# Kernel optimization log

Hardware: AMD Instinct MI355X
Metric: run time of the kernel (lower is better)

## Reference

```python
import jax, jax.numpy as jnp
import numpy as np

V, EMB, H, N, E, B = 100000, 300, 64, 20000, 160000, 4096
L, T = 2, 3  # layer_timesteps = [3, 3]


def setup_inputs() -> dict:
    key = jax.random.key(0)
    ks = jax.random.split(key, 24)
    ri = lambda k, shape, hi: jax.random.randint(k, shape, 0, hi)
    rn = lambda k, shape, s=0.05: (jax.random.normal(k, shape, dtype=jnp.float32) * s)
    emb_table = rn(ks[7], (V, EMB), 0.1).at[0].set(0.0)  # padding_idx=0 row is zeros
    return {
        'emb_ind0': ri(ks[0], (N,), V),
        'emb_ind1': ri(ks[1], (N,), V),
        'adj0': ri(ks[2], (E, 2), N),
        'adj1': ri(ks[3], (E, 2), N),
        'prop_ind0': ri(ks[4], (B,), N),
        'prop_ind1': ri(ks[5], (B,), N),
        'labels': ri(ks[6], (B,), 2),
        'emb_table': emb_table,
        'proj_W': rn(ks[8], (EMB, H)),   # emb_proj weight (stored input-major)
        'proj_b': jnp.zeros((H,), jnp.float32),
        'msg_W': rn(ks[9], (L, H, H)),   # per-layer edge-type-0 message linear
        'msg_b': jnp.zeros((L, H), jnp.float32),
        'gru_Wih': rn(ks[10], (L, 3 * H, H)),
        'gru_Whh': rn(ks[11], (L, 3 * H, H)),
        'gru_bih': jnp.zeros((L, 3 * H), jnp.float32),
        'gru_bhh': jnp.zeros((L, 3 * H), jnp.float32),
        'cla_W1': rn(ks[12], (2 * H, 16)),
        'cla_b1': jnp.zeros((16,), jnp.float32),
        'cla_W2': rn(ks[13], (16, 1)),
        'cla_b2': jnp.zeros((1,), jnp.float32),
    }


def _gru_cell(x, h, Wih, Whh, bih, bhh):
    # torch.nn.GRUCell math
    gi = x @ Wih.T + bih
    gh = h @ Whh.T + bhh
    i_r, i_z, i_n = jnp.split(gi, 3, axis=-1)
    h_r, h_z, h_n = jnp.split(gh, 3, axis=-1)
    r = jax.nn.sigmoid(i_r + h_r)
    z = jax.nn.sigmoid(i_z + h_z)
    n = jnp.tanh(i_n + r * h_n)
    return (1.0 - z) * n + z * h


def reference(emb_ind0, emb_ind1, adj0, adj1, prop_ind0, prop_ind1, labels,
              emb_table, proj_W, proj_b, msg_W, msg_b,
              gru_Wih, gru_Whh, gru_bih, gru_bhh,
              cla_W1, cla_b1, cla_W2, cla_b2):
    def ggnn(x, adj):
        src, tgt = adj[:, 0], adj[:, 1]
        h = x
        for l in range(L):              # 2 structurally distinct layers
            for _ in range(T):          # 3 timesteps each
                m = h[src] @ msg_W[l] + msg_b[l]                     # [E, H] gather + transform
                inc = jax.ops.segment_sum(m, tgt, num_segments=N)    # scatter-add messages
                h = _gru_cell(inc, h, gru_Wih[l], gru_Whh[l], gru_bih[l], gru_bhh[l])
        return h

    def branch(emb_ind, adj, prop_ind):
        ge = emb_table[emb_ind]          # embedding lookup [N, EMB]
        ge = ge @ proj_W + proj_b        # emb_proj -> [N, H]
        ge = ggnn(ge, adj)
        return ge[prop_ind]              # index_select -> [B, H]

    g0 = branch(emb_ind0, adj0, prop_ind0)
    g1 = branch(emb_ind1, adj1, prop_ind1)
    ge = jnp.concatenate([g0, g1], axis=-1)                 # match='concat' -> [B, 2H]
    hid = jax.nn.relu(ge @ cla_W1 + cla_b1)
    logits = jax.nn.sigmoid(hid @ cla_W2 + cla_b2)          # [B, 1], num_class=1 path
    p = logits.squeeze(-1)
    y = labels.astype(p.dtype)
    eps = 1e-7  # mirrors torch BCELoss log-clamping
    loss = -jnp.mean(y * jnp.log(jnp.clip(p, eps, 1.0))
                     + (1.0 - y) * jnp.log(jnp.clip(1.0 - p, eps, 1.0)))
    return logits, loss
```

## Files before the change

kernel.cpp:

```cpp
#include <hip/hip_runtime.h>
#include <hip/hip_bf16.h>

typedef unsigned short u16;
typedef __attribute__((ext_vector_type(8))) short s16x8;
typedef __attribute__((ext_vector_type(4))) float f32x4;

#define NN 20000
#define HH 64
#define EMBD 300
#define EE 160000
#define BB 4096
#define NODES 40000
#define SLST  640000

#define OFF_PROJB 0
#define OFF_MSGB  64
#define OFF_BIH   192
#define OFF_BHH   576
#define OFF_CW1T  960
#define OFF_CB1   3008
#define OFF_CW2   3024
#define OFF_CB2   3040
#define PARAM_SZ  3072

#define PB_WIH   0
#define PB_WHH   24576
#define PB_WMT   49152
#define PB_PROJT 57344
#define PB_SZ    77824

#define APAD 344

__device__ __forceinline__ float b2f(u16 u) {
    union { unsigned int i; float f; } v; v.i = ((unsigned int)u) << 16; return v.f;
}
__device__ __forceinline__ u16 f2b(float f) {
    union { float f; unsigned int u; } v; v.f = f;
    unsigned int u = v.u;
    return (u16)((u + 0x7FFFu + ((u >> 16) & 1u)) >> 16);
}
__device__ __forceinline__ float ldf(const void* p, long long i, int isbf) {
    return isbf ? b2f(((const u16*)p)[i]) : ((const float*)p)[i];
}
__device__ __forceinline__ u16 ldb(const void* p, long long i, int isbf) {
    return isbf ? ((const u16*)p)[i] : f2b(((const float*)p)[i]);
}
__device__ __forceinline__ void stf(void* p, long long i, int isbf, float v) {
    if (isbf) ((u16*)p)[i] = f2b(v);
    else      ((float*)p)[i] = v;
}

__global__ void sniff_kernel(const u16* probe, int* flag)
{
    if (threadIdx.x == 0 && blockIdx.x == 0) {
        int good = 0;
        for (int i = 0; i < 128; i += 2) {
            unsigned int e = (probe[i] >> 7) & 0xFF;
            if (e >= 105 && e <= 127) good++;
        }
        *flag = (good >= 48) ? 1 : 0;
    }
}

__global__ __launch_bounds__(256) void conv_kernel(
    const void* projW, const void* projb, const void* msgW, const void* msgb,
    const void* wih, const void* whh, const void* bih, const void* bhh,
    const void* cw1, const void* cb1, const void* cw2, const void* cb2,
    float* P, u16* PB, const int* flag)
{
    int isbf = *flag;
    int i = blockIdx.x * 256 + threadIdx.x;
    if (i < 64)    P[OFF_PROJB + i] = ldf(projb, i, isbf);
    if (i < 128)   P[OFF_MSGB + i]  = ldf(msgb, i, isbf);
    if (i < 384)   { P[OFF_BIH + i] = ldf(bih, i, isbf); P[OFF_BHH + i] = ldf(bhh, i, isbf); }
    if (i < 2048)  { int t = i >> 7, k = i & 127; P[OFF_CW1T + i] = ldf(cw1, (long long)k * 16 + t, isbf); }
    if (i < 16)    { P[OFF_CB1 + i] = ldf(cb1, i, isbf); P[OFF_CW2 + i] = ldf(cw2, i, isbf); }
    if (i == 0)    P[OFF_CB2] = ldf(cb2, 0, isbf);

    if (i < 24576) {
        int l = i / 12288, r = i - l * 12288;
        int frag = r >> 9, rr = r & 511, lane = rr >> 3, e = rr & 7;
        int jt = frag >> 1, kt = frag & 1;
        int srow = jt * 16 + (lane & 15);
        int sk = kt * 32 + ((lane >> 4) << 3) + e;
        long long si = (long long)l * 12288 + srow * 64 + sk;
        PB[PB_WIH + i] = ldb(wih, si, isbf);
        PB[PB_WHH + i] = ldb(whh, si, isbf);
    }
    if (i < 8192) {
        int l = i >> 12, r = i & 4095;
        int frag = r >> 9, rr = r & 511, lane = rr >> 3, e = rr & 7;
        int jt = frag >> 1, kt = frag & 1;
        int srow = jt * 16 + (lane & 15);
        int sk = kt * 32 + ((lane >> 4) << 3) + e;
        PB[PB_WMT + i] = ldb(msgW, (long long)l * 4096 + sk * 64 + srow, isbf);
    }
    if (i < 20480) {
        int frag = i >> 9, rr = i & 511, lane = rr >> 3, e = rr & 7;
        int jt = frag / 10, kt = frag - jt * 10;
        int srow = jt * 16 + (lane & 15);
        int sk = kt * 32 + ((lane >> 4) << 3) + e;
        PB[PB_PROJT + i] = (sk < 300) ? ldb(projW, (long long)sk * 64 + srow, isbf) : (u16)0;
    }
}

__global__ __launch_bounds__(256) void hist_kernel(const int* __restrict__ adj0,
                                                   const int* __restrict__ adj1, int* off)
{
    int e = blockIdx.x * 256 + threadIdx.x;
    if (e >= 2 * EE) return;
    int b = e / EE, le = e - b * EE;
    const int* adj = b ? adj1 : adj0;
    int tgt = adj[2 * le + 1];
    atomicAdd(&off[b * (NN + 1) + tgt + 1], 1);
}

__global__ __launch_bounds__(1024) void scan_kernel(int* off, int* cursor)
{
    int b = blockIdx.x;
    int* o = off + (size_t)b * (NN + 1);
    int* cur = cursor + (size_t)b * NN;
    __shared__ int wsum[16];
    __shared__ int wscan[16];
    int tid = threadIdx.x, wv = tid >> 6, lane = tid & 63;
    int base = 0;
    for (int start = 0; start < NN; start += 1024) {
        int i = start + tid;
        int v = (i < NN) ? o[i + 1] : 0;
        int orig = v;
        #pragma unroll
        for (int d = 1; d < 64; d <<= 1) {
            int t = __shfl_up(v, d);
            if (lane >= d) v += t;
        }
        if (lane == 63) wsum[wv] = v;
        __syncthreads();
        if (tid < 16) {
            int w = wsum[tid];
            #pragma unroll
            for (int d = 1; d < 16; d <<= 1) {
                int t = __shfl_up(w, d, 16);
                if (tid >= d) w += t;
            }
            wscan[tid] = w;
        }
        __syncthreads();
        int woff = (wv == 0) ? 0 : wscan[wv - 1];
        int excl = base + woff + v - orig;
        if (i < NN) { o[i] = excl; cur[i] = excl; }
        base += wscan[15];
    }
    if (tid == 0) o[NN] = base;
}

__global__ __launch_bounds__(256) void scatter_kernel(const int* __restrict__ adj0,
                                                      const int* __restrict__ adj1,
                                                      int* cursor, int* esrc)
{
    int e = blockIdx.x * 256 + threadIdx.x;
    if (e >= 2 * EE) return;
    int b = e / EE, le = e - b * EE;
    const int* adj = b ? adj1 : adj0;
    int src = adj[2 * le + 0];
    int tgt = adj[2 * le + 1];
    int pos = atomicAdd(&cursor[b * NN + tgt], 1);
    esrc[(size_t)b * EE + pos] = src;
}

__global__ __launch_bounds__(256) void projm_kernel(const void* emb,
                                                    const int* __restrict__ i0,
                                                    const int* __restrict__ i1,
                                                    const float* __restrict__ P,
                                                    const u16* __restrict__ PB,
                                                    u16* __restrict__ h, const int* flag)
{
    __shared__ u16 sA[64 * APAD];
    int isbf = *flag;
    int tid = threadIdx.x;
    int node0 = blockIdx.x * 64;

    {
        int r = tid >> 2, sub = tid & 3;
        int n = node0 + r;
        int b = n >= NN;
        int ln = n - b * NN;
        int idx = b ? i1[ln] : i0[ln];
        if (isbf) {
            const ushort4* src = (const ushort4*)((const u16*)emb + (size_t)idx * EMBD);
            ushort4* dst = (ushort4*)(sA + r * APAD);
            for (int c = sub; c < 75; c += 4) dst[c] = src[c];
            if (sub == 0) {
                ushort4 z = {0, 0, 0, 0};
                for (int c = 75; c < 80; ++c) dst[c] = z;
            }
        } else {
            const float* src = (const float*)emb + (size_t)idx * EMBD;
            for (int k = sub; k < 300; k += 4) sA[r * APAD + k] = f2b(src[k]);
            if (sub == 0) for (int k = 300; k < 320; ++k) sA[r * APAD + k] = 0;
        }
    }

    int wv = tid >> 6, lane = tid & 63, quad = lane >> 4, cn = lane & 15;
    int m0 = wv * 16;
    f32x4 acc[4];
    #pragma unroll
    for (int j = 0; j < 4; ++j) {
        float bb = P[OFF_PROJB + j * 16 + cn];
        acc[j] = {bb, bb, bb, bb};
    }
    #pragma unroll
    for (int kt = 0; kt < 10; ++kt) {
        s16x8 a = *(const s16x8*)&sA[(m0 + cn) * APAD + kt * 32 + quad * 8];
        #pragma unroll
        for (int j = 0; j < 4; ++j) {
            s16x8 bfr = *(const s16x8*)&PB[PB_PROJT + (j * 10 + kt) * 512 + lane * 8];
            acc[j] = __builtin_amdgcn_mfma_f32_16x16x32_bf16(a, bfr, acc[j], 0, 0, 0);
        }
    }
    #pragma unroll
    for (int j = 0; j < 4; ++j)
        #pragma unroll
        for (int r = 0; r < 4; ++r)
            h[(size_t)j * SLST + (size_t)(node0 + m0 + quad * 4 + r) * 16 + cn] = f2b(acc[j][r]);
}

__global__ __launch_bounds__(256) void gatherS_kernel(const u16* __restrict__ h_old,
                                                      u16* __restrict__ Sbuf,
                                                      const int* __restrict__ ioff,
                                                      const int* __restrict__ esrc)
{
    int b = blockIdx.x;
    int slice = b & 3;
    int tile = b >> 2;
    int tid = threadIdx.x;
    int i = tid >> 4, feat = tid & 15;
    int node = tile * 16 + i;
    int br = node >= NN;
    int ln = node - br * NN;
    const int* o = ioff + (size_t)br * (NN + 1);
    int s0 = o[ln], s1 = o[ln + 1];
    const int* es = esrc + (size_t)br * EE;
    const u16* hb = h_old + (size_t)slice * SLST + (size_t)br * NN * 16;
    float a0 = 0.f, a1 = 0.f, a2 = 0.f, a3 = 0.f;
    int e = s0;
    for (; e + 4 <= s1; e += 4) {
        int e0 = es[e], e1 = es[e + 1], e2 = es[e + 2], e3 = es[e + 3];
        a0 += b2f(hb[(size_t)e0 * 16 + feat]);
        a1 += b2f(hb[(size_t)e1 * 16 + feat]);
        a2 += b2f(hb[(size_t)e2 * 16 + feat]);
        a3 += b2f(hb[(size_t)e3 * 16 + feat]);
    }
    for (; e < s1; ++e) a0 += b2f(hb[(size_t)es[e] * 16 + feat]);
    Sbuf[(size_t)slice * SLST + (size_t)node * 16 + feat] = f2b(a0 + a1 + a2 + a3);
}

__global__ __launch_bounds__(256) void gstep_kernel(const u16* __restrict__ Sbuf,
                                                    const u16* __restrict__ h_old,
                                                    u16* __restrict__ h_new,
                                                    const int* __restrict__ ioff,
                                                    const float* __restrict__ P,
                                                    const u16* __restrict__ PB, int l)
{
    __shared__ u16 s_S[4096];
    __shared__ u16 s_h[4096];
    __shared__ float s_deg[64];

    int tid = threadIdx.x;
    int wv = tid >> 6, lane = tid & 63;
    int node0 = blockIdx.x * 64;
    int m0 = wv * 16;

    #pragma unroll
    for (int it = 0; it < 2; ++it) {
        int idx = it * 64 + lane;
        int slice = idx >> 5;
        int rem = idx & 31;
        int nlo = rem >> 1, half = rem & 1;
        int row = m0 + nlo;
        size_t goff = (size_t)slice * SLST + (size_t)(node0 + row) * 16 + half * 8;
        *(uint4*)(s_h + row * 64 + slice * 16 + half * 8) = *(const uint4*)(h_old + goff);
        *(uint4*)(s_S + row * 64 + slice * 16 + half * 8) = *(const uint4*)(Sbuf + goff);
    }
    if (lane < 16) {
        int row = m0 + lane;
        int n = node0 + row;
        int br = n >= NN;
        int ln = n - br * NN;
        const int* o = ioff + (size_t)br * (NN + 1);
        s_deg[row] = (float)(o[ln + 1] - o[ln]);
    }

    int quad = lane >> 4, cn = lane & 15;
    int arow = (m0 + cn) * 64 + quad * 8;
    int fl = lane * 8;

    s16x8 aS0 = *(const s16x8*)&s_S[arow];
    s16x8 aS1 = *(const s16x8*)&s_S[arow + 32];
    const u16* WM = PB + PB_WMT + (size_t)l * 4096;
    #pragma unroll
    for (int jt = 0; jt < 4; ++jt) {
        float mb = P[OFF_MSGB + l * 64 + jt * 16 + cn];
        f32x4 acc;
        acc[0] = s_deg[m0 + quad * 4 + 0] * mb;
        acc[1] = s_deg[m0 + quad * 4 + 1] * mb;
        acc[2] = s_deg[m0 + quad * 4 + 2] * mb;
        acc[3] = s_deg[m0 + quad * 4 + 3] * mb;
        acc = __builtin_amdgcn_mfma_f32_16x16x32_bf16(aS0, *(const s16x8*)&WM[(jt * 2 + 0) * 512 + fl], acc, 0, 0, 0);
        acc = __builtin_amdgcn_mfma_f32_16x16x32_bf16(aS1, *(const s16x8*)&WM[(jt * 2 + 1) * 512 + fl], acc, 0, 0, 0);
        #pragma unroll
        for (int r = 0; r < 4; ++r)
            s_S[(m0 + quad * 4 + r) * 64 + jt * 16 + cn] = f2b(acc[r]);
    }

    s16x8 aI0 = *(const s16x8*)&s_S[arow];
    s16x8 aI1 = *(const s16x8*)&s_S[arow + 32];
    s16x8 aH0 = *(const s16x8*)&s_h[arow];
    s16x8 aH1 = *(const s16x8*)&s_h[arow + 32];
    const u16* WI = PB + PB_WIH + (size_t)l * 12288;
    const u16* WH = PB + PB_WHH + (size_t)l * 12288;
    const float* bi = P + OFF_BIH + l * 192;
    const float* bh = P + OFF_BHH + l * 192;

    #pragma unroll
    for (int c = 0; c < 4; ++c) {
        int j0 = c * 16;
        float vr = bi[j0 + cn], vz = bi[64 + j0 + cn], vn = bi[128 + j0 + cn];
        float wr = bh[j0 + cn], wz = bh[64 + j0 + cn], wn = bh[128 + j0 + cn];
        f32x4 gr = {vr, vr, vr, vr}, gz = {vz, vz, vz, vz}, gn = {vn, vn, vn, vn};
        f32x4 hr = {wr, wr, wr, wr}, hz = {wz, wz, wz, wz}, hn = {wn, wn, wn, wn};
        int fr = (c * 2) * 512 + fl, frz = ((4 + c) * 2) * 512 + fl, frn = ((8 + c) * 2) * 512 + fl;
        gr = __builtin_amdgcn_mfma_f32_16x16x32_bf16(aI0, *(const s16x8*)&WI[fr], gr, 0, 0, 0);
        gr = __builtin_amdgcn_mfma_f32_16x16x32_bf16(aI1, *(const s16x8*)&WI[fr + 512], gr, 0, 0, 0);
        gz = __builtin_amdgcn_mfma_f32_16x16x32_bf16(aI0, *(const s16x8*)&WI[frz], gz, 0, 0, 0);
        gz = __builtin_amdgcn_mfma_f32_16x16x32_bf16(aI1, *(const s16x8*)&WI[frz + 512], gz, 0, 0, 0);
        gn = __builtin_amdgcn_mfma_f32_16x16x32_bf16(aI0, *(const s16x8*)&WI[frn], gn, 0, 0, 0);
        gn = __builtin_amdgcn_mfma_f32_16x16x32_bf16(aI1, *(const s16x8*)&WI[frn + 512], gn, 0, 0, 0);
        hr = __builtin_amdgcn_mfma_f32_16x16x32_bf16(aH0, *(const s16x8*)&WH[fr], hr, 0, 0, 0);
        hr = __builtin_amdgcn_mfma_f32_16x16x32_bf16(aH1, *(const s16x8*)&WH[fr + 512], hr, 0, 0, 0);
        hz = __builtin_amdgcn_mfma_f32_16x16x32_bf16(aH0, *(const s16x8*)&WH[frz], hz, 0, 0, 0);
        hz = __builtin_amdgcn_mfma_f32_16x16x32_bf16(aH1, *(const s16x8*)&WH[frz + 512], hz, 0, 0, 0);
        hn = __builtin_amdgcn_mfma_f32_16x16x32_bf16(aH0, *(const s16x8*)&WH[frn], hn, 0, 0, 0);
        hn = __builtin_amdgcn_mfma_f32_16x16x32_bf16(aH1, *(const s16x8*)&WH[frn + 512], hn, 0, 0, 0);
        #pragma unroll
        for (int r = 0; r < 4; ++r) {
            int row = m0 + quad * 4 + r;
            float rr = 1.f / (1.f + __expf(-(gr[r] + hr[r])));
            float zz = 1.f / (1.f + __expf(-(gz[r] + hz[r])));
            float nn = tanhf(gn[r] + rr * hn[r]);
            float ho = b2f(s_h[row * 64 + j0 + cn]);
            h_new[(size_t)c * SLST + (size_t)(node0 + row) * 16 + cn] = f2b((1.f - zz) * nn + zz * ho);
        }
    }
}

__global__ __launch_bounds__(256) void cls_kernel(const u16* __restrict__ h,
                                                  const int* __restrict__ p0,
                                                  const int* __restrict__ p1,
                                                  const int* __restrict__ labels,
                                                  const float* __restrict__ P,
                                                  void* out, float* partial, const int* flag)
{
    int isbf = *flag;
    int wv = threadIdx.x >> 6, lane = threadIdx.x & 63;
    int s = blockIdx.x * 4 + wv;
    int n0 = p0[s], n1 = p1[s];
    size_t sl = (size_t)(lane >> 4) * SLST;
    float f0 = b2f(h[sl + (size_t)n0 * 16 + (lane & 15)]);
    float f1 = b2f(h[sl + (size_t)(NN + n1) * 16 + (lane & 15)]);
    float z = P[OFF_CB2];
    #pragma unroll
    for (int t = 0; t < 16; ++t) {
        float part = f0 * P[OFF_CW1T + t * 128 + lane] + f1 * P[OFF_CW1T + t * 128 + 64 + lane];
        #pragma unroll
        for (int off = 32; off; off >>= 1) part += __shfl_xor(part, off);
        z += fmaxf(part + P[OFF_CB1 + t], 0.f) * P[OFF_CW2 + t];
    }
    float p = 1.f / (1.f + expf(-z));
    float y = (float)labels[s];
    const float eps = 1e-7f;
    float pc  = fminf(fmaxf(p, eps), 1.f);
    float pc1 = fminf(fmaxf(1.f - p, eps), 1.f);
    float term = y * logf(pc) + (1.f - y) * logf(pc1);
    __shared__ float red[4];
    if (lane == 0) { stf(out, s, isbf, p); red[wv] = term; }
    __syncthreads();
    if (threadIdx.x == 0) partial[blockIdx.x] = red[0] + red[1] + red[2] + red[3];
}

__global__ __launch_bounds__(256) void loss_kernel(const float* __restrict__ partial,
                                                   void* out, const int* flag)
{
    __shared__ float red[256];
    int tid = threadIdx.x;
    float s = 0.f;
    for (int i = tid; i < 1024; i += 256) s += partial[i];
    red[tid] = s;
    __syncthreads();
    for (int d = 128; d > 0; d >>= 1) {
        if (tid < d) red[tid] += red[tid + d];
        __syncthreads();
    }
    if (tid == 0) stf(out, BB, *flag, -red[0] / (float)BB);
}

extern "C" void kernel_launch(void* const* d_in, const int* in_sizes, int n_in,
                              void* d_out, int out_size, void* d_ws, size_t ws_size,
                              hipStream_t stream)
{
    const int* adj0   = (const int*)d_in[2];
    const int* adj1   = (const int*)d_in[3];
    const int* prop0  = (const int*)d_in[4];
    const int* prop1  = (const int*)d_in[5];
    const int* labels = (const int*)d_in[6];

    int* flag = (int*)d_ws;
    float* P  = (float*)d_ws + 16;
    u16* PB   = (u16*)(P + PARAM_SZ);
    u16* h0   = PB + PB_SZ;
    u16* h1   = h0 + (size_t)4 * SLST / 4 * 4;
    u16* SB   = h1 + (size_t)2560000;
    float* partial = (float*)(SB + (size_t)2560000);
    int* ioff   = (int*)(partial + 1024);
    int* cursor = ioff + 2 * (NN + 1) + 62;
    int* esrc   = cursor + 2 * NN;

    hipMemsetAsync(ioff, 0, 2 * (NN + 1) * sizeof(int), stream);

    sniff_kernel<<<1, 64, 0, stream>>>((const u16*)d_in[8], flag);
    conv_kernel<<<96, 256, 0, stream>>>(d_in[8], d_in[9], d_in[10], d_in[11], d_in[12], d_in[13],
                                        d_in[14], d_in[15], d_in[16], d_in[17], d_in[18], d_in[19],
                                        P, PB, flag);
    hist_kernel<<<(2 * EE) / 256, 256, 0, stream>>>(adj0, adj1, ioff);
    scan_kernel<<<2, 1024, 0, stream>>>(ioff, cursor);
    scatter_kernel<<<(2 * EE) / 256, 256, 0, stream>>>(adj0, adj1, cursor, esrc);
    projm_kernel<<<(2 * NN) / 64, 256, 0, stream>>>(d_in[7], (const int*)d_in[0],
                                                    (const int*)d_in[1], P, PB, h0, flag);

    u16* hcur = h0;
    u16* hnext = h1;
    for (int l = 0; l < 2; ++l) {
        for (int t = 0; t < 3; ++t) {
            gatherS_kernel<<<4 * (NODES / 16), 256, 0, stream>>>(hcur, SB, ioff, esrc);
            gstep_kernel<<<NODES / 64, 256, 0, stream>>>(SB, hcur, hnext, ioff, P, PB, l);
            u16* tmp = hcur; hcur = hnext; hnext = tmp;
        }
    }

    cls_kernel<<<BB / 4, 256, 0, stream>>>(hcur, prop0, prop1, labels, P, d_out, partial, flag);
    loss_kernel<<<1, 256, 0, stream>>>(partial, d_out, flag);
}
```

Before: 464.8 us.

## Widen node-state slices to 32 features, stage GRU weights in LDS, fold memset

Node hidden states move from four 16-feature slices to two 32-feature slices, so each gathered neighbour row is a 64-byte read instead of 32 bytes, which halves the number of scattered gather transactions per edge. The gstep kernel now copies the per-layer Wih, Whh and message weights into shared memory before its MFMAs, and replaces tanhf with an exp-based formula. The hipMemset of the offset array is folded into the conversion kernel. The cost is about 57 KB of extra LDS per block, which lowers occupancy, plus a redundant weight copy in every block.

```diff
diff --git a/kernel.cpp b/kernel.cpp
--- a/kernel.cpp
+++ b/kernel.cpp
@@ -11,7 +11,7 @@
 #define EE 160000
 #define BB 4096
 #define NODES 40000
-#define SLST  640000
+#define SLST2 1280000
 
 #define OFF_PROJB 0
 #define OFF_MSGB  64
@@ -29,6 +29,10 @@
 #define PB_PROJT 57344
 #define PB_SZ    77824
 
+#define WIH_S 0
+#define WHH_S 12288
+#define WMT_S 24576
+
 #define APAD 344
 
 __device__ __forceinline__ float b2f(u16 u) {
@@ -66,10 +70,11 @@
     const void* projW, const void* projb, const void* msgW, const void* msgb,
     const void* wih, const void* whh, const void* bih, const void* bhh,
     const void* cw1, const void* cb1, const void* cw2, const void* cb2,
-    float* P, u16* PB, const int* flag)
+    float* P, u16* PB, int* ioff, const int* flag)
 {
     int isbf = *flag;
     int i = blockIdx.x * 256 + threadIdx.x;
+    if (i < 2 * (NN + 1)) ioff[i] = 0;
     if (i < 64)    P[OFF_PROJB + i] = ldf(projb, i, isbf);
     if (i < 128)   P[OFF_MSGB + i]  = ldf(msgb, i, isbf);
     if (i < 384)   { P[OFF_BIH + i] = ldf(bih, i, isbf); P[OFF_BHH + i] = ldf(bhh, i, isbf); }
@@ -221,7 +226,8 @@
     for (int j = 0; j < 4; ++j)
         #pragma unroll
         for (int r = 0; r < 4; ++r)
-            h[(size_t)j * SLST + (size_t)(node0 + m0 + quad * 4 + r) * 16 + cn] = f2b(acc[j][r]);
+            h[(size_t)(j >> 1) * SLST2 + (size_t)(node0 + m0 + quad * 4 + r) * 32
+              + (j & 1) * 16 + cn] = f2b(acc[j][r]);
 }
 
 __global__ __launch_bounds__(256) void gatherS_kernel(const u16* __restrict__ h_old,
@@ -230,28 +236,28 @@
                                                       const int* __restrict__ esrc)
 {
     int b = blockIdx.x;
-    int slice = b & 3;
-    int tile = b >> 2;
+    int slice = b & 1;
+    int tile = b >> 1;
     int tid = threadIdx.x;
-    int i = tid >> 4, feat = tid & 15;
-    int node = tile * 16 + i;
+    int i = tid >> 5, feat = tid & 31;
+    int node = tile * 8 + i;
     int br = node >= NN;
     int ln = node - br * NN;
     const int* o = ioff + (size_t)br * (NN + 1);
     int s0 = o[ln], s1 = o[ln + 1];
     const int* es = esrc + (size_t)br * EE;
-    const u16* hb = h_old + (size_t)slice * SLST + (size_t)br * NN * 16;
+    const u16* hb = h_old + (size_t)slice * SLST2 + (size_t)br * NN * 32;
     float a0 = 0.f, a1 = 0.f, a2 = 0.f, a3 = 0.f;
     int e = s0;
     for (; e + 4 <= s1; e += 4) {
         int e0 = es[e], e1 = es[e + 1], e2 = es[e + 2], e3 = es[e + 3];
-        a0 += b2f(hb[(size_t)e0 * 16 + feat]);
-        a1 += b2f(hb[(size_t)e1 * 16 + feat]);
-        a2 += b2f(hb[(size_t)e2 * 16 + feat]);
-        a3 += b2f(hb[(size_t)e3 * 16 + feat]);
-    }
-    for (; e < s1; ++e) a0 += b2f(hb[(size_t)es[e] * 16 + feat]);
-    Sbuf[(size_t)slice * SLST + (size_t)node * 16 + feat] = f2b(a0 + a1 + a2 + a3);
+        a0 += b2f(hb[(size_t)e0 * 32 + feat]);
+        a1 += b2f(hb[(size_t)e1 * 32 + feat]);
+        a2 += b2f(hb[(size_t)e2 * 32 + feat]);
+        a3 += b2f(hb[(size_t)e3 * 32 + feat]);
+    }
+    for (; e < s1; ++e) a0 += b2f(hb[(size_t)es[e] * 32 + feat]);
+    Sbuf[(size_t)slice * SLST2 + (size_t)node * 32 + feat] = f2b(a0 + a1 + a2 + a3);
 }
 
 __global__ __launch_bounds__(256) void gstep_kernel(const u16* __restrict__ Sbuf,
@@ -261,6 +267,7 @@
                                                     const float* __restrict__ P,
                                                     const u16* __restrict__ PB, int l)
 {
+    __shared__ u16 s_W[28672];
     __shared__ u16 s_S[4096];
     __shared__ u16 s_h[4096];
     __shared__ float s_deg[64];
@@ -270,16 +277,25 @@
     int node0 = blockIdx.x * 64;
     int m0 = wv * 16;
 
+    {
+        const uint4* a = (const uint4*)(PB + PB_WIH + (size_t)l * 12288);
+        const uint4* bq = (const uint4*)(PB + PB_WHH + (size_t)l * 12288);
+        uint4* da = (uint4*)(s_W + WIH_S);
+        uint4* db = (uint4*)(s_W + WHH_S);
+        for (int i = tid; i < 1536; i += 256) { da[i] = a[i]; db[i] = bq[i]; }
+        const uint4* cq = (const uint4*)(PB + PB_WMT + (size_t)l * 4096);
+        uint4* dc = (uint4*)(s_W + WMT_S);
+        for (int i = tid; i < 512; i += 256) dc[i] = cq[i];
+    }
+
     #pragma unroll
     for (int it = 0; it < 2; ++it) {
-        int idx = it * 64 + lane;
-        int slice = idx >> 5;
-        int rem = idx & 31;
-        int nlo = rem >> 1, half = rem & 1;
-        int row = m0 + nlo;
-        size_t goff = (size_t)slice * SLST + (size_t)(node0 + row) * 16 + half * 8;
-        *(uint4*)(s_h + row * 64 + slice * 16 + half * 8) = *(const uint4*)(h_old + goff);
-        *(uint4*)(s_S + row * 64 + slice * 16 + half * 8) = *(const uint4*)(Sbuf + goff);
+        int c = it * 64 + lane;
+        int row = c >> 3, q = c & 7;
+        int slice = q >> 2, part = q & 3;
+        size_t goff = (size_t)slice * SLST2 + (size_t)(node0 + m0 + row) * 32 + part * 8;
+        *(uint4*)(s_h + (m0 + row) * 64 + slice * 32 + part * 8) = *(const uint4*)(h_old + goff);
+        *(uint4*)(s_S + (m0 + row) * 64 + slice * 32 + part * 8) = *(const uint4*)(Sbuf + goff);
     }
     if (lane < 16) {
         int row = m0 + lane;
@@ -289,6 +305,7 @@
         const int* o = ioff + (size_t)br * (NN + 1);
         s_deg[row] = (float)(o[ln + 1] - o[ln]);
     }
+    __syncthreads();
 
     int quad = lane >> 4, cn = lane & 15;
     int arow = (m0 + cn) * 64 + quad * 8;
@@ -296,7 +313,6 @@
 
     s16x8 aS0 = *(const s16x8*)&s_S[arow];
     s16x8 aS1 = *(const s16x8*)&s_S[arow + 32];
-    const u16* WM = PB + PB_WMT + (size_t)l * 4096;
     #pragma unroll
     for (int jt = 0; jt < 4; ++jt) {
         float mb = P[OFF_MSGB + l * 64 + jt * 16 + cn];
@@ -305,8 +321,8 @@
         acc[1] = s_deg[m0 + quad * 4 + 1] * mb;
         acc[2] = s_deg[m0 + quad * 4 + 2] * mb;
         acc[3] = s_deg[m0 + quad * 4 + 3] * mb;
-        acc = __builtin_amdgcn_mfma_f32_16x16x32_bf16(aS0, *(const s16x8*)&WM[(jt * 2 + 0) * 512 + fl], acc, 0, 0, 0);
-        acc = __builtin_amdgcn_mfma_f32_16x16x32_bf16(aS1, *(const s16x8*)&WM[(jt * 2 + 1) * 512 + fl], acc, 0, 0, 0);
+        acc = __builtin_amdgcn_mfma_f32_16x16x32_bf16(aS0, *(const s16x8*)&s_W[WMT_S + (jt * 2 + 0) * 512 + fl], acc, 0, 0, 0);
+        acc = __builtin_amdgcn_mfma_f32_16x16x32_bf16(aS1, *(const s16x8*)&s_W[WMT_S + (jt * 2 + 1) * 512 + fl], acc, 0, 0, 0);
         #pragma unroll
         for (int r = 0; r < 4; ++r)
             s_S[(m0 + quad * 4 + r) * 64 + jt * 16 + cn] = f2b(acc[r]);
@@ -316,8 +332,6 @@
     s16x8 aI1 = *(const s16x8*)&s_S[arow + 32];
     s16x8 aH0 = *(const s16x8*)&s_h[arow];
     s16x8 aH1 = *(const s16x8*)&s_h[arow + 32];
-    const u16* WI = PB + PB_WIH + (size_t)l * 12288;
-    const u16* WH = PB + PB_WHH + (size_t)l * 12288;
     const float* bi = P + OFF_BIH + l * 192;
     const float* bh = P + OFF_BHH + l * 192;
 
@@ -328,27 +342,35 @@
         float wr = bh[j0 + cn], wz = bh[64 + j0 + cn], wn = bh[128 + j0 + cn];
         f32x4 gr = {vr, vr, vr, vr}, gz = {vz, vz, vz, vz}, gn = {vn, vn, vn, vn};
         f32x4 hr = {wr, wr, wr, wr}, hz = {wz, wz, wz, wz}, hn = {wn, wn, wn, wn};
-        int fr = (c * 2) * 512 + fl, frz = ((4 + c) * 2) * 512 + fl, frn = ((8 + c) * 2) * 512 + fl;
-        gr = __builtin_amdgcn_mfma_f32_16x16x32_bf16(aI0, *(const s16x8*)&WI[fr], gr, 0, 0, 0);
-        gr = __builtin_amdgcn_mfma_f32_16x16x32_bf16(aI1, *(const s16x8*)&WI[fr + 512], gr, 0, 0, 0);
-        gz = __builtin_amdgcn_mfma_f32_16x16x32_bf16(aI0, *(const s16x8*)&WI[frz], gz, 0, 0, 0);
-        gz = __builtin_amdgcn_mfma_f32_16x16x32_bf16(aI1, *(const s16x8*)&WI[frz + 512], gz, 0, 0, 0);
-        gn = __builtin_amdgcn_mfma_f32_16x16x32_bf16(aI0, *(const s16x8*)&WI[frn], gn, 0, 0, 0);
-        gn = __builtin_amdgcn_mfma_f32_16x16x32_bf16(aI1, *(const s16x8*)&WI[frn + 512], gn, 0, 0, 0);
-        hr = __builtin_amdgcn_mfma_f32_16x16x32_bf16(aH0, *(const s16x8*)&WH[fr], hr, 0, 0, 0);
-        hr = __builtin_amdgcn_mfma_f32_16x16x32_bf16(aH1, *(const s16x8*)&WH[fr + 512], hr, 0, 0, 0);
-        hz = __builtin_amdgcn_mfma_f32_16x16x32_bf16(aH0, *(const s16x8*)&WH[frz], hz, 0, 0, 0);
-        hz = __builtin_amdgcn_mfma_f32_16x16x32_bf16(aH1, *(const s16x8*)&WH[frz + 512], hz, 0, 0, 0);
-        hn = __builtin_amdgcn_mfma_f32_16x16x32_bf16(aH0, *(const s16x8*)&WH[frn], hn, 0, 0, 0);
-        hn = __builtin_amdgcn_mfma_f32_16x16x32_bf16(aH1, *(const s16x8*)&WH[frn + 512], hn, 0, 0, 0);
+        int fr  = WIH_S + (c * 2) * 512 + fl;
+        int frz = WIH_S + ((4 + c) * 2) * 512 + fl;
+        int frn = WIH_S + ((8 + c) * 2) * 512 + fl;
+        int hrr = WHH_S + (c * 2) * 512 + fl;
+        int hrz = WHH_S + ((4 + c) * 2) * 512 + fl;
+        int hrn = WHH_S + ((8 + c) * 2) * 512 + fl;
+        gr = __builtin_amdgcn_mfma_f32_16x16x32_bf16(aI0, *(const s16x8*)&s_W[fr], gr, 0, 0, 0);
+        gr = __builtin_amdgcn_mfma_f32_16x16x32_bf16(aI1, *(const s16x8*)&s_W[fr + 512], gr, 0, 0, 0);
+        gz = __builtin_amdgcn_mfma_f32_16x16x32_bf16(aI0, *(const s16x8*)&s_W[frz], gz, 0, 0, 0);
+        gz = __builtin_amdgcn_mfma_f32_16x16x32_bf16(aI1, *(const s16x8*)&s_W[frz + 512], gz, 0, 0, 0);
+        gn = __builtin_amdgcn_mfma_f32_16x16x32_bf16(aI0, *(const s16x8*)&s_W[frn], gn, 0, 0, 0);
+        gn = __builtin_amdgcn_mfma_f32_16x16x32_bf16(aI1, *(const s16x8*)&s_W[frn + 512], gn, 0, 0, 0);
+        hr = __builtin_amdgcn_mfma_f32_16x16x32_bf16(aH0, *(const s16x8*)&s_W[hrr], hr, 0, 0, 0);
+        hr = __builtin_amdgcn_mfma_f32_16x16x32_bf16(aH1, *(const s16x8*)&s_W[hrr + 512], hr, 0, 0, 0);
+        hz = __builtin_amdgcn_mfma_f32_16x16x32_bf16(aH0, *(const s16x8*)&s_W[hrz], hz, 0, 0, 0);
+        hz = __builtin_amdgcn_mfma_f32_16x16x32_bf16(aH1, *(const s16x8*)&s_W[hrz + 512], hz, 0, 0, 0);
+        hn = __builtin_amdgcn_mfma_f32_16x16x32_bf16(aH0, *(const s16x8*)&s_W[hrn], hn, 0, 0, 0);
+        hn = __builtin_amdgcn_mfma_f32_16x16x32_bf16(aH1, *(const s16x8*)&s_W[hrn + 512], hn, 0, 0, 0);
         #pragma unroll
         for (int r = 0; r < 4; ++r) {
             int row = m0 + quad * 4 + r;
             float rr = 1.f / (1.f + __expf(-(gr[r] + hr[r])));
             float zz = 1.f / (1.f + __expf(-(gz[r] + hz[r])));
-            float nn = tanhf(gn[r] + rr * hn[r]);
+            float xx = gn[r] + rr * hn[r];
+            float tv = __expf(-2.f * fabsf(xx));
+            float nn = __builtin_copysignf((1.f - tv) / (1.f + tv), xx);
             float ho = b2f(s_h[row * 64 + j0 + cn]);
-            h_new[(size_t)c * SLST + (size_t)(node0 + row) * 16 + cn] = f2b((1.f - zz) * nn + zz * ho);
+            h_new[(size_t)(c >> 1) * SLST2 + (size_t)(node0 + row) * 32 + (c & 1) * 16 + cn]
+                = f2b((1.f - zz) * nn + zz * ho);
         }
     }
 }
@@ -364,15 +386,16 @@
     int wv = threadIdx.x >> 6, lane = threadIdx.x & 63;
     int s = blockIdx.x * 4 + wv;
     int n0 = p0[s], n1 = p1[s];
-    size_t sl = (size_t)(lane >> 4) * SLST;
-    float f0 = b2f(h[sl + (size_t)n0 * 16 + (lane & 15)]);
-    float f1 = b2f(h[sl + (size_t)(NN + n1) * 16 + (lane & 15)]);
+    size_t sl = (size_t)(lane >> 5) * SLST2;
+    int off = lane & 31;
+    float f0 = b2f(h[sl + (size_t)n0 * 32 + off]);
+    float f1 = b2f(h[sl + (size_t)(NN + n1) * 32 + off]);
     float z = P[OFF_CB2];
     #pragma unroll
     for (int t = 0; t < 16; ++t) {
         float part = f0 * P[OFF_CW1T + t * 128 + lane] + f1 * P[OFF_CW1T + t * 128 + 64 + lane];
         #pragma unroll
-        for (int off = 32; off; off >>= 1) part += __shfl_xor(part, off);
+        for (int o2 = 32; o2; o2 >>= 1) part += __shfl_xor(part, o2);
         z += fmaxf(part + P[OFF_CB1 + t], 0.f) * P[OFF_CW2 + t];
     }
     float p = 1.f / (1.f + expf(-z));
@@ -417,30 +440,28 @@
     float* P  = (float*)d_ws + 16;
     u16* PB   = (u16*)(P + PARAM_SZ);
     u16* h0   = PB + PB_SZ;
-    u16* h1   = h0 + (size_t)4 * SLST / 4 * 4;
-    u16* SB   = h1 + (size_t)2560000;
-    float* partial = (float*)(SB + (size_t)2560000);
+    u16* h1   = h0 + (size_t)2 * SLST2;
+    u16* SB   = h1 + (size_t)2 * SLST2;
+    float* partial = (float*)(SB + (size_t)2 * SLST2);
     int* ioff   = (int*)(partial + 1024);
     int* cursor = ioff + 2 * (NN + 1) + 62;
     int* esrc   = cursor + 2 * NN;
 
-    hipMemsetAsync(ioff, 0, 2 * (NN + 1) * sizeof(int), stream);
-
     sniff_kernel<<<1, 64, 0, stream>>>((const u16*)d_in[8], flag);
-    conv_kernel<<<96, 256, 0, stream>>>(d_in[8], d_in[9], d_in[10], d_in[11], d_in[12], d_in[13],
-                                        d_in[14], d_in[15], d_in[16], d_in[17], d_in[18], d_in[19],
-                                        P, PB, flag);
+    conv_kernel<<<157, 256, 0, stream>>>(d_in[8], d_in[9], d_in[10], d_in[11], d_in[12], d_in[13],
+                                         d_in[14], d_in[15], d_in[16], d_in[17], d_in[18], d_in[19],
+                                         P, PB, ioff, flag);
     hist_kernel<<<(2 * EE) / 256, 256, 0, stream>>>(adj0, adj1, ioff);
     scan_kernel<<<2, 1024, 0, stream>>>(ioff, cursor);
     scatter_kernel<<<(2 * EE) / 256, 256, 0, stream>>>(adj0, adj1, cursor, esrc);
-    projm_kernel<<<(2 * NN) / 64, 256, 0, stream>>>(d_in[7], (const int*)d_in[0],
-                                                    (const int*)d_in[1], P, PB, h0, flag);
+    projm_kernel<<<NODES / 64, 256, 0, stream>>>(d_in[7], (const int*)d_in[0],
+                                                 (const int*)d_in[1], P, PB, h0, flag);
 
     u16* hcur = h0;
     u16* hnext = h1;
     for (int l = 0; l < 2; ++l) {
         for (int t = 0; t < 3; ++t) {
-            gatherS_kernel<<<4 * (NODES / 16), 256, 0, stream>>>(hcur, SB, ioff, esrc);
+            gatherS_kernel<<<2 * (NODES / 8), 256, 0, stream>>>(hcur, SB, ioff, esrc);
             gstep_kernel<<<NODES / 64, 256, 0, stream>>>(SB, hcur, hnext, ioff, P, PB, l);
             u16* tmp = hcur; hcur = hnext; hnext = tmp;
         }
```

Measured after the change: 479.7 us. 3.2% more time.
